# Kernel tuning notes

Measured on AMD Instinct MI355X. Metric: run time of the kernel, lower is better.

## Reference

```python
import jax, jax.numpy as jnp
import numpy as np

B, Hm, Wm, Dm = 1, 32, 32, 32
N = Hm * Wm * Dm
C = 128
HEADS, DH = 8, 16
G = 32
L = 2
OUT = 1


def _ln(x, g, b):
    mu = jnp.mean(x, -1, keepdims=True)
    var = jnp.mean((x - mu) ** 2, -1, keepdims=True)
    return (x - mu) * jax.lax.rsqrt(var + 1e-5) * g + b


def setup_inputs() -> dict:
    key = jax.random.key(0)
    ks = iter(jax.random.split(key, 64))
    def nrm(shape, s=0.02):
        return jax.random.normal(next(ks), shape, jnp.float32) * s
    return {
        "x": jax.random.normal(next(ks), (B, N, 3), jnp.float32),
        "fx": jax.random.normal(next(ks), (B, N, 1), jnp.float32),
        "pre_w1": nrm((4, 2 * C)), "pre_b1": jnp.zeros((2 * C,), jnp.float32),
        "pre_w2": nrm((2 * C, C)), "pre_b2": jnp.zeros((C,), jnp.float32),
        "placeholder": jax.random.uniform(next(ks), (C,), jnp.float32) / C,
        "ln1_g": jnp.ones((L, C), jnp.float32), "ln1_b": jnp.zeros((L, C), jnp.float32),
        "convx_w": nrm((L, C, C, 3, 3, 3)), "convx_b": jnp.zeros((L, C), jnp.float32),
        "convfx_w": nrm((L, C, C, 3, 3, 3)), "convfx_b": jnp.zeros((L, C), jnp.float32),
        "slice_w": nrm((L, DH, G), 0.1), "slice_b": jnp.zeros((L, G), jnp.float32),
        "temperature": jnp.full((L, 1, HEADS, 1, 1), 0.5, jnp.float32),
        "wq": nrm((L, DH, DH), 0.1), "wk": nrm((L, DH, DH), 0.1), "wv": nrm((L, DH, DH), 0.1),
        "wo": nrm((L, HEADS * DH, C)), "bo": jnp.zeros((L, C), jnp.float32),
        "ln2_g": jnp.ones((L, C), jnp.float32), "ln2_b": jnp.zeros((L, C), jnp.float32),
        "mlp_w1": nrm((L, C, C)), "mlp_b1": jnp.zeros((L, C), jnp.float32),
        "mlp_w2": nrm((L, C, C)), "mlp_b2": jnp.zeros((L, C), jnp.float32),
        "ln3_g": jnp.ones((C,), jnp.float32), "ln3_b": jnp.zeros((C,), jnp.float32),
        "out_w": nrm((C, OUT)), "out_b": jnp.zeros((OUT,), jnp.float32),
    }


def _conv3d(x, w, b):
    # x: [B,C,H,W,D], w: [O,I,3,3,3], SAME padding (kernel//2) as torch Conv3d
    y = jax.lax.conv_general_dilated(x, w, (1, 1, 1), "SAME",
                                     dimension_numbers=("NCDHW", "OIDHW", "NCDHW"))
    return y + b[None, :, None, None, None]


def _physics_attn(z, cw_x, cb_x, cw_fx, cb_fx, sw, sb, temp, wq, wk, wv, wo, bo):
    # z: [B, N, C] -> structured mesh conv projections -> slice attention
    xg = z.reshape(B, Hm, Wm, Dm, C).transpose(0, 4, 1, 2, 3)  # [B,C,H,W,D]

    def split_heads(t):  # [B,I,H,W,D] -> [B,heads,N,dh]
        return t.transpose(0, 2, 3, 4, 1).reshape(B, N, HEADS, DH).transpose(0, 2, 1, 3)

    x_mid = split_heads(_conv3d(xg, cw_x, cb_x))
    fx_mid = split_heads(_conv3d(xg, cw_fx, cb_fx))
    # slice assignment weights: [B,heads,N,G], temperature-scaled softmax
    slice_logits = (x_mid @ sw + sb) / temp
    swt = jax.nn.softmax(slice_logits, axis=-1)
    norm = jnp.sum(swt, axis=2)  # [B,heads,G]
    tok = jnp.einsum("bhnc,bhng->bhgc", fx_mid, swt) / (norm + 1e-5)[..., None]
    q, k, v = tok @ wq, tok @ wk, tok @ wv  # [B,heads,G,dh]
    attn = jax.nn.softmax((q @ k.transpose(0, 1, 3, 2)) * (DH ** -0.5), axis=-1)
    ot = attn @ v  # [B,heads,G,dh]
    out = jnp.einsum("bhgc,bhng->bhnc", ot, swt)  # de-slice back to tokens
    out = out.transpose(0, 2, 1, 3).reshape(B, N, HEADS * DH)
    return out @ wo + bo


def reference(x, fx, pre_w1, pre_b1, pre_w2, pre_b2, placeholder,
              ln1_g, ln1_b, convx_w, convx_b, convfx_w, convfx_b,
              slice_w, slice_b, temperature, wq, wk, wv, wo, bo,
              ln2_g, ln2_b, mlp_w1, mlp_b1, mlp_w2, mlp_b2,
              ln3_g, ln3_b, out_w, out_b):
    h = jnp.concatenate([x, fx], axis=-1)  # [B,N,space+fun]
    z = jax.nn.gelu(h @ pre_w1 + pre_b1, approximate=False) @ pre_w2 + pre_b2 + placeholder
    for l in range(L):
        zn = _ln(z, ln1_g[l], ln1_b[l])
        z = _physics_attn(zn, convx_w[l], convx_b[l], convfx_w[l], convfx_b[l],
                          slice_w[l], slice_b[l], temperature[l],
                          wq[l], wk[l], wv[l], wo[l], bo[l]) + z
        zn = _ln(z, ln2_g[l], ln2_b[l])
        z = jax.nn.gelu(zn @ mlp_w1[l] + mlp_b1[l], approximate=False) @ mlp_w2[l] + mlp_b2[l] + z
    return _ln(z, ln3_g, ln3_b) @ out_w + out_b
```

## Files before the change

kernel.cpp:

```cpp
#include <hip/hip_runtime.h>
#include <hip/hip_bf16.h>

#define DEV __device__ __forceinline__

constexpr int N   = 32768;
constexpr int TOTAL_IN = 2038481;

constexpr int OFF_X        = 0;
constexpr int OFF_FX       = 98304;
constexpr int OFF_PRE_W1   = 131072;
constexpr int OFF_PRE_B1   = 132096;
constexpr int OFF_PRE_W2   = 132352;
constexpr int OFF_PRE_B2   = 165120;
constexpr int OFF_PLACE    = 165248;
constexpr int OFF_LN1_G    = 165376;
constexpr int OFF_LN1_B    = 165632;
constexpr int OFF_CONVX_W  = 165888;
constexpr int OFF_CONVX_B  = 1050624;
constexpr int OFF_CONVFX_W = 1050880;
constexpr int OFF_CONVFX_B = 1935616;
constexpr int OFF_SLICE_W  = 1935872;
constexpr int OFF_SLICE_B  = 1936896;
constexpr int OFF_TEMP     = 1936960;
constexpr int OFF_WQ       = 1936976;
constexpr int OFF_WK       = 1937488;
constexpr int OFF_WV       = 1938000;
constexpr int OFF_WO       = 1938512;
constexpr int OFF_BO       = 1971280;
constexpr int OFF_LN2_G    = 1971536;
constexpr int OFF_LN2_B    = 1971792;
constexpr int OFF_MLP_W1   = 1972048;
constexpr int OFF_MLP_B1   = 2004816;
constexpr int OFF_MLP_W2   = 2005072;
constexpr int OFF_MLP_B2   = 2037840;
constexpr int OFF_LN3_G    = 2038096;
constexpr int OFF_LN3_B    = 2038224;
constexpr int OFF_OUT_W    = 2038352;
constexpr int OFF_OUT_B    = 2038480;

__device__ __constant__ int d_PRE[32] = {
  0, 98304, 131072, 132096, 132352, 165120, 165248, 165376, 165632,
  165888, 1050624, 1050880, 1935616, 1935872, 1936896, 1936960, 1936976,
  1937488, 1938000, 1938512, 1971280, 1971536, 1971792, 1972048, 2004816,
  2005072, 2037840, 2038096, 2038224, 2038352, 2038480, 2038481
};

constexpr size_t F_IN   = 16;
constexpr size_t F_WT   = 2038512;
constexpr size_t F_Z    = F_WT   + 1769472;
constexpr size_t F_ZN   = F_Z    + 4194304;
constexpr size_t F_CONV = F_ZN   + 4194304;
constexpr size_t F_SWT  = F_CONV + 8388608;
constexpr size_t F_TOKP = F_SWT  + 8388608;
constexpr size_t F_TOKR = F_TOKP + 1114112;
constexpr size_t F_OT   = F_TOKR + 4352;
constexpr size_t F_WP   = F_OT   + 4096;
constexpr size_t F_END  = F_WP   + 65536;

struct InPtrs { const void* p[31]; };

typedef short short8v  __attribute__((ext_vector_type(8)));
typedef float float4v  __attribute__((ext_vector_type(4)));
#define MFMA16(A,B,C) __builtin_amdgcn_mfma_f32_16x16x32_bf16(A,B,C,0,0,0)

DEV float geluf(float x) { return 0.5f * x * (1.0f + erff(x * 0.70710678118654752f)); }
DEV short f2bs(float x) { union { __hip_bfloat16 h; short s; } c; c.h = __float2bfloat16(x); return c.s; }

__global__ void k_convert(InPtrs ptrs, float* __restrict__ ws) {
  const unsigned tw = *(const unsigned*)ptrs.p[15];
  const bool isbf = (tw == 0x3F003F00u);
  int stride = gridDim.x * blockDim.x;
  for (int e = blockIdx.x * blockDim.x + threadIdx.x; e < TOTAL_IN; e += stride) {
    int lo = 0, hi = 30;
#pragma unroll
    for (int it = 0; it < 5; ++it) {
      int mid = (lo + hi + 1) >> 1;
      if (e >= d_PRE[mid]) lo = mid; else hi = mid - 1;
    }
    int loc = e - d_PRE[lo];
    float v;
    if (isbf) {
      unsigned short u = ((const unsigned short*)ptrs.p[lo])[loc];
      unsigned uu = ((unsigned)u) << 16;
      v = __uint_as_float(uu);
    } else {
      v = ((const float*)ptrs.p[lo])[loc];
    }
    ws[F_IN + e] = v;
  }
}

__global__ void k_wtrans(const float* __restrict__ ip, short* __restrict__ wtf) {
  int f = blockIdx.x * 256 + threadIdx.x;
  if (f >= 221184) return;
  int lane = f & 63;
  int rest = f >> 6;
  int ntile = rest & 15;
  int r2 = rest >> 4;
  int layer = r2 / 108;
  int kt = r2 - layer * 108;
  int icb = kt / 27, tap = kt - icb * 27;
  int oc = ntile * 16 + (lane & 15);
  int ic0 = icb * 32 + (lane >> 4) * 8;
  const float* cw = ip + (oc < 128 ? OFF_CONVX_W : OFF_CONVFX_W);
  int o = oc & 127;
  const float* src = cw + ((size_t)(layer * 128 + o) * 128) * 27 + tap;
  short8v out;
#pragma unroll
  for (int j = 0; j < 8; ++j) out[j] = f2bs(src[(ic0 + j) * 27]);
  *(short8v*)(wtf + (size_t)f * 8) = out;
}

__global__ void k_wpack(const float* __restrict__ ip, short* __restrict__ wp) {
  int f = blockIdx.x * 256 + threadIdx.x;
  if (f >= 16384) return;
  int lane = f & 63;
  int t = f >> 6;
  int srcoff, kt, nt;
  if (t < 64) { srcoff = OFF_PRE_W2; kt = t >> 3; nt = t & 7; }
  else {
    int r = t - 64, l = r / 96, r2 = r - l * 96;
    int which = r2 >> 5, idx2 = r2 & 31;
    kt = idx2 >> 3; nt = idx2 & 7;
    srcoff = (which == 0 ? OFF_MLP_W1 : (which == 1 ? OFF_MLP_W2 : OFF_WO)) + l * 16384;
  }
  int k0 = kt * 32 + (lane >> 4) * 8;
  int n = nt * 16 + (lane & 15);
  const float* src = ip + srcoff + (size_t)k0 * 128 + n;
  short8v out;
#pragma unroll
  for (int j = 0; j < 8; ++j) out[j] = f2bs(src[(size_t)j * 128]);
  *(short8v*)(wp + (size_t)f * 8) = out;
}

__global__ __launch_bounds__(256)
void k_prenet(const float* __restrict__ ip, const short* __restrict__ wp, float* __restrict__ z) {
  __shared__ float w1s[1024], b1s[256], cvec[128];
  __shared__ float xv[64][4];
  __shared__ __align__(16) short ts[64 * 264];
  int tid = threadIdx.x;
  int wv = tid >> 6, lane = tid & 63;
  int m = lane & 15, q = lane >> 4;
  int n0 = blockIdx.x * 64;
  for (int i = tid; i < 1024; i += 256) w1s[i] = ip[OFF_PRE_W1 + i];
  b1s[tid] = ip[OFF_PRE_B1 + tid];
  if (tid < 128) cvec[tid] = ip[OFF_PRE_B2 + tid] + ip[OFF_PLACE + tid];
  if (tid < 64) {
    xv[tid][0] = ip[OFF_X + (n0 + tid) * 3 + 0];
    xv[tid][1] = ip[OFF_X + (n0 + tid) * 3 + 1];
    xv[tid][2] = ip[OFF_X + (n0 + tid) * 3 + 2];
    xv[tid][3] = ip[OFF_FX + n0 + tid];
  }
  __syncthreads();
  {
    float w0 = w1s[tid], wA = w1s[256 + tid], wB = w1s[512 + tid], wC = w1s[768 + tid];
    float bb = b1s[tid];
    for (int t = 0; t < 64; ++t) {
      float hv = bb + xv[t][0] * w0 + xv[t][1] * wA + xv[t][2] * wB + xv[t][3] * wC;
      ts[t * 264 + tid] = f2bs(geluf(hv));
    }
  }
  __syncthreads();
  const short8v* pwf = (const short8v*)wp;
  float4v acc[8];
#pragma unroll
  for (int nt = 0; nt < 8; ++nt) acc[nt] = (float4v){0.f, 0.f, 0.f, 0.f};
  for (int kt = 0; kt < 8; ++kt) {
    short8v A = *(const short8v*)(ts + (wv * 16 + m) * 264 + kt * 32 + q * 8);
#pragma unroll
    for (int nt = 0; nt < 8; ++nt)
      acc[nt] = MFMA16(A, pwf[(kt * 8 + nt) * 64 + lane], acc[nt]);
  }
#pragma unroll
  for (int nt = 0; nt < 8; ++nt) {
    int col = nt * 16 + m;
#pragma unroll
    for (int r = 0; r < 4; ++r)
      z[(size_t)(n0 + wv * 16 + q * 4 + r) * 128 + col] = acc[nt][r] + cvec[col];
  }
}

__global__ void k_ln_bf(const float* __restrict__ src, short* __restrict__ dst,
                        const float* __restrict__ gm, const float* __restrict__ bt) {
  int wv = threadIdx.x >> 6, lane = threadIdx.x & 63;
  int n = blockIdx.x * 4 + wv;
  const float2 v = *(const float2*)&src[(size_t)n * 128 + lane * 2];
  float s1 = v.x + v.y, s2 = v.x * v.x + v.y * v.y;
#pragma unroll
  for (int off = 32; off; off >>= 1) { s1 += __shfl_xor(s1, off); s2 += __shfl_xor(s2, off); }
  float mu = s1 * (1.0f / 128.0f);
  float var = s2 * (1.0f / 128.0f) - mu * mu;
  float rst = 1.0f / sqrtf(var + 1e-5f);
  const float2 g2 = *(const float2*)&gm[lane * 2];
  const float2 b2 = *(const float2*)&bt[lane * 2];
  union { short s[2]; unsigned u; } c;
  c.s[0] = f2bs((v.x - mu) * rst * g2.x + b2.x);
  c.s[1] = f2bs((v.y - mu) * rst * g2.y + b2.y);
  *(unsigned*)&dst[(size_t)n * 128 + lane * 2] = c.u;
}

__global__ __launch_bounds__(256)
void k_conv(const float* __restrict__ ip, const short* __restrict__ znb,
            const short* __restrict__ wtf, float* __restrict__ cv, int layer) {
  __shared__ __align__(16) short halo[16320];
  int tid = threadIdx.x;
  int wv = tid >> 6, lane = tid & 63;
  int m = lane & 15, q = lane >> 4;
  int n0 = blockIdx.x * 64;
  int h = n0 >> 10, w0 = (n0 >> 5) & 31;
  float bias_r[4];
#pragma unroll
  for (int nt = 0; nt < 4; ++nt) {
    int oc = (wv * 4 + nt) * 16 + m;
    bias_r[nt] = (oc < 128) ? ip[OFF_CONVX_B + layer * 128 + oc]
                            : ip[OFF_CONVFX_B + layer * 128 + (oc - 128)];
  }
  float4v acc[4][4];
#pragma unroll
  for (int a = 0; a < 4; ++a)
#pragma unroll
    for (int b = 0; b < 4; ++b) acc[a][b] = (float4v){0.f, 0.f, 0.f, 0.f};

  const short8v* wf = (const short8v*)wtf + (size_t)layer * 110592 + (wv * 4) * 64 + lane;
  const int laneA = m * 40 + q * 8;
  short8v bc0 = wf[0], bc1 = wf[64], bc2 = wf[128], bc3 = wf[192];

  int tap = 0, icb = 0;
  for (int kt = 0; kt < 108; ++kt) {
    if (tap == 0) {
      __syncthreads();
      for (int i = tid; i < 1632; i += 256) {
        int pr = i >> 2, qq = i & 3;
        int line = pr / 34, dpos = pr - line * 34;
        int hh2 = h + (line >> 2) - 1, ww2 = w0 + (line & 3) - 1, dd2 = dpos - 1;
        short8v v = (short8v){0, 0, 0, 0, 0, 0, 0, 0};
        if (((unsigned)hh2 < 32u) && ((unsigned)ww2 < 32u) && ((unsigned)dd2 < 32u)) {
          int tok = (hh2 << 10) + (ww2 << 5) + dd2;
          v = *(const short8v*)(znb + (size_t)tok * 128 + icb * 32 + qq * 8);
        }
        *(short8v*)(halo + pr * 40 + qq * 8) = v;
      }
      __syncthreads();
    }
    int ktn = (kt + 1 < 108) ? kt + 1 : kt;
    const short8v* wn = wf + (size_t)ktn * 1024;
    short8v bn0 = wn[0], bn1 = wn[64], bn2 = wn[128], bn3 = wn[192];

    int ta = tap / 9, rem = tap - ta * 9, tb = rem / 3, tc = rem - tb * 3;
    const short* hp = halo + ((ta * 4 + tb) * 34 + tc) * 40 + laneA;
    short8v A0 = *(const short8v*)(hp);
    short8v A1 = *(const short8v*)(hp + 640);
    short8v A2 = *(const short8v*)(hp + 1360);
    short8v A3 = *(const short8v*)(hp + 2000);

    acc[0][0] = MFMA16(A0, bc0, acc[0][0]);
    acc[1][0] = MFMA16(A1, bc0, acc[1][0]);
    acc[2][0] = MFMA16(A2, bc0, acc[2][0]);
    acc[3][0] = MFMA16(A3, bc0, acc[3][0]);
    acc[0][1] = MFMA16(A0, bc1, acc[0][1]);
    acc[1][1] = MFMA16(A1, bc1, acc[1][1]);
    acc[2][1] = MFMA16(A2, bc1, acc[2][1]);
    acc[3][1] = MFMA16(A3, bc1, acc[3][1]);
    acc[0][2] = MFMA16(A0, bc2, acc[0][2]);
    acc[1][2] = MFMA16(A1, bc2, acc[1][2]);
    acc[2][2] = MFMA16(A2, bc2, acc[2][2]);
    acc[3][2] = MFMA16(A3, bc2, acc[3][2]);
    acc[0][3] = MFMA16(A0, bc3, acc[0][3]);
    acc[1][3] = MFMA16(A1, bc3, acc[1][3]);
    acc[2][3] = MFMA16(A2, bc3, acc[2][3]);
    acc[3][3] = MFMA16(A3, bc3, acc[3][3]);

    bc0 = bn0; bc1 = bn1; bc2 = bn2; bc3 = bn3;
    if (++tap == 27) { tap = 0; ++icb; }
  }
#pragma unroll
  for (int mt = 0; mt < 4; ++mt) {
    float* cp = cv + (size_t)(n0 + mt * 16 + q * 4) * 256 + (wv * 4) * 16 + m;
#pragma unroll
    for (int nt = 0; nt < 4; ++nt) {
#pragma unroll
      for (int r = 0; r < 4; ++r)
        cp[(size_t)r * 256 + nt * 16] = acc[mt][nt][r] + bias_r[nt];
    }
  }
}

__global__ __launch_bounds__(256)
void k_slice(const float* __restrict__ ip, const float* __restrict__ cv,
             short* __restrict__ swtb, float* __restrict__ tokp, int layer) {
  __shared__ float sws[512], sbs[32], its[8];
  __shared__ float swl[32 * 257];
  __shared__ float fxl[32 * 128];
  int tid = threadIdx.x;
  for (int i = tid; i < 512; i += 256) sws[i] = ip[OFF_SLICE_W + layer * 512 + i];
  if (tid < 32) sbs[tid] = ip[OFF_SLICE_B + layer * 32 + tid];
  if (tid < 8)  its[tid] = 1.0f / ip[OFF_TEMP + layer * 8 + tid];
  float4 ta0 = make_float4(0,0,0,0), ta1 = ta0, ta2 = ta0, ta3 = ta0;
  float np = 0.f;
  for (int s = 0; s < 4; ++s) {
    int tbase = blockIdx.x * 128 + s * 32;
    __syncthreads();
    for (int i = tid; i < 1024; i += 256) {
      int t = i >> 5, c4 = (i & 31) * 4;
      *(float4*)&fxl[t * 128 + c4] = *(const float4*)&cv[(size_t)(tbase + t) * 256 + 128 + c4];
    }
    {
      int t = tid >> 3, hh = tid & 7;
      float xm[16];
#pragma unroll
      for (int qq = 0; qq < 4; ++qq)
        *(float4*)&xm[qq * 4] = *(const float4*)&cv[(size_t)(tbase + t) * 256 + hh * 16 + qq * 4];
      float lg[32];
      float itv = its[hh];
#pragma unroll
      for (int g = 0; g < 32; ++g) {
        float sacc = sbs[g];
#pragma unroll
        for (int j = 0; j < 16; ++j) sacc += xm[j] * sws[j * 32 + g];
        lg[g] = sacc * itv;
      }
      float mx = -1e30f;
#pragma unroll
      for (int g = 0; g < 32; ++g) mx = fmaxf(mx, lg[g]);
      float sum = 0.f;
#pragma unroll
      for (int g = 0; g < 32; ++g) { lg[g] = expf(lg[g] - mx); sum += lg[g]; }
      float inv = 1.0f / sum;
#pragma unroll
      for (int g = 0; g < 32; ++g) {
        lg[g] *= inv;
        swl[t * 257 + hh * 32 + g] = lg[g];
      }
#pragma unroll
      for (int qq = 0; qq < 4; ++qq) {
        short8v pk;
#pragma unroll
        for (int j = 0; j < 8; ++j) pk[j] = f2bs(lg[qq * 8 + j]);
        *(short8v*)(swtb + (size_t)(tbase + t) * 256 + hh * 32 + qq * 8) = pk;
      }
    }
    __syncthreads();
    {
      int ah = tid >> 5, ag = tid & 31;
      for (int t2 = 0; t2 < 32; ++t2) {
        float sv = swl[t2 * 257 + ah * 32 + ag];
        np += sv;
        const float* f = &fxl[t2 * 128 + ah * 16];
        float4 f0 = *(const float4*)&f[0], f1 = *(const float4*)&f[4];
        float4 f2 = *(const float4*)&f[8], f3 = *(const float4*)&f[12];
        ta0.x += sv * f0.x; ta0.y += sv * f0.y; ta0.z += sv * f0.z; ta0.w += sv * f0.w;
        ta1.x += sv * f1.x; ta1.y += sv * f1.y; ta1.z += sv * f1.z; ta1.w += sv * f1.w;
        ta2.x += sv * f2.x; ta2.y += sv * f2.y; ta2.z += sv * f2.z; ta2.w += sv * f2.w;
        ta3.x += sv * f3.x; ta3.y += sv * f3.y; ta3.z += sv * f3.z; ta3.w += sv * f3.w;
      }
    }
  }
  int ah = tid >> 5, ag = tid & 31;
  size_t base = (size_t)blockIdx.x * 4352 + (size_t)(ah * 32 + ag) * 16;
  *(float4*)&tokp[base + 0]  = ta0;
  *(float4*)&tokp[base + 4]  = ta1;
  *(float4*)&tokp[base + 8]  = ta2;
  *(float4*)&tokp[base + 12] = ta3;
  tokp[(size_t)blockIdx.x * 4352 + 4096 + ah * 32 + ag] = np;
}

__global__ void k_tokred(const float* __restrict__ tokp, float* __restrict__ tokr) {
  int o = blockIdx.x * 256 + threadIdx.x;
  if (o < 4352) {
    float s = 0.f;
    for (int b = 0; b < 256; ++b) s += tokp[(size_t)b * 4352 + o];
    tokr[o] = s;
  }
}

__global__ __launch_bounds__(256)
void k_attn(const float* __restrict__ ip, const float* __restrict__ tokr,
            float* __restrict__ ot, int layer) {
  __shared__ float kk[256 * 17], vv[256 * 17];
  int tid = threadIdx.x;
  int hh = tid >> 5;
  const float* wq = ip + OFF_WQ + layer * 256;
  const float* wk = ip + OFF_WK + layer * 256;
  const float* wv = ip + OFF_WV + layer * 256;
  float inv = 1.0f / (tokr[4096 + tid] + 1e-5f);
  float t[16];
#pragma unroll
  for (int c = 0; c < 16; ++c) t[c] = tokr[tid * 16 + c] * inv;
  float q[16];
#pragma unroll
  for (int c = 0; c < 16; ++c) {
    float aq = 0.f, ak = 0.f, av = 0.f;
#pragma unroll
    for (int j = 0; j < 16; ++j) {
      float tv = t[j];
      aq += tv * wq[j * 16 + c];
      ak += tv * wk[j * 16 + c];
      av += tv * wv[j * 16 + c];
    }
    q[c] = aq;
    kk[tid * 17 + c] = ak;
    vv[tid * 17 + c] = av;
  }
  __syncthreads();
  float sc[32];
  float mx = -1e30f;
#pragma unroll
  for (int g2 = 0; g2 < 32; ++g2) {
    float s = 0.f;
#pragma unroll
    for (int c = 0; c < 16; ++c) s += q[c] * kk[(hh * 32 + g2) * 17 + c];
    s *= 0.25f;
    sc[g2] = s; mx = fmaxf(mx, s);
  }
  float sum = 0.f;
#pragma unroll
  for (int g2 = 0; g2 < 32; ++g2) { sc[g2] = expf(sc[g2] - mx); sum += sc[g2]; }
  float inv2 = 1.0f / sum;
  float o[16];
#pragma unroll
  for (int c = 0; c < 16; ++c) o[c] = 0.f;
#pragma unroll
  for (int g2 = 0; g2 < 32; ++g2) {
    float p = sc[g2] * inv2;
#pragma unroll
    for (int c = 0; c < 16; ++c) o[c] += p * vv[(hh * 32 + g2) * 17 + c];
  }
#pragma unroll
  for (int c = 0; c < 16; ++c) ot[tid * 16 + c] = o[c];
}

__global__ __launch_bounds__(256)
void k_out(const float* __restrict__ ip, const short* __restrict__ swtb,
           const float* __restrict__ ot, const short* __restrict__ wp,
           float* __restrict__ z, int layer) {
  __shared__ __align__(16) short otb[8 * 512];
  __shared__ __align__(16) short al[64 * 136];
  __shared__ float bol[128];
  int tid = threadIdx.x;
  int wv = tid >> 6, lane = tid & 63;
  int m = lane & 15, q = lane >> 4;
  int n0 = blockIdx.x * 64;
  if (tid < 128) bol[tid] = ip[OFF_BO + layer * 128 + tid];
  for (int i = tid; i < 4096; i += 256) {
    int h = i >> 9, r = i & 511, ln = r >> 3, j = r & 7;
    int g = (ln >> 4) * 8 + j, dh = ln & 15;
    otb[i] = f2bs(ot[h * 512 + g * 16 + dh]);
  }
  __syncthreads();
  float4v accd[8];
#pragma unroll
  for (int h = 0; h < 8; ++h) accd[h] = (float4v){0.f, 0.f, 0.f, 0.f};
#pragma unroll
  for (int h = 0; h < 8; ++h) {
    short8v A = *(const short8v*)(swtb + (size_t)(n0 + wv * 16 + m) * 256 + h * 32 + q * 8);
    accd[h] = MFMA16(A, *(const short8v*)(otb + h * 512 + lane * 8), accd[h]);
  }
#pragma unroll
  for (int h = 0; h < 8; ++h)
#pragma unroll
    for (int r = 0; r < 4; ++r)
      al[(wv * 16 + q * 4 + r) * 136 + h * 16 + m] = f2bs(accd[h][r]);
  __syncthreads();
  const short8v* wof = (const short8v*)(wp + (size_t)(128 + 96 * layer) * 512);
  float4v a2[8];
#pragma unroll
  for (int nt = 0; nt < 8; ++nt) a2[nt] = (float4v){0.f, 0.f, 0.f, 0.f};
  for (int kt = 0; kt < 4; ++kt) {
    short8v A = *(const short8v*)(al + (wv * 16 + m) * 136 + kt * 32 + q * 8);
#pragma unroll
    for (int nt = 0; nt < 8; ++nt)
      a2[nt] = MFMA16(A, wof[(kt * 8 + nt) * 64 + lane], a2[nt]);
  }
#pragma unroll
  for (int nt = 0; nt < 8; ++nt) {
    int col = nt * 16 + m;
#pragma unroll
    for (int r = 0; r < 4; ++r) {
      size_t zi = (size_t)(n0 + wv * 16 + q * 4 + r) * 128 + col;
      z[zi] += a2[nt][r] + bol[col];
    }
  }
}

__global__ __launch_bounds__(256)
void k_mlp(const float* __restrict__ ip, const short* __restrict__ znb,
           const short* __restrict__ wp, float* __restrict__ z, int layer) {
  __shared__ __align__(16) short znt[64 * 136];
  __shared__ __align__(16) short hid[64 * 136];
  __shared__ float b1s[128], b2s[128];
  int tid = threadIdx.x;
  int wv = tid >> 6, lane = tid & 63;
  int m = lane & 15, q = lane >> 4;
  int n0 = blockIdx.x * 64;
  if (tid < 128) {
    b1s[tid] = ip[OFF_MLP_B1 + layer * 128 + tid];
    b2s[tid] = ip[OFF_MLP_B2 + layer * 128 + tid];
  }
  for (int i = tid; i < 1024; i += 256) {
    int row = i >> 4, c8 = (i & 15) * 8;
    *(short8v*)(znt + row * 136 + c8) = *(const short8v*)(znb + (size_t)(n0 + row) * 128 + c8);
  }
  __syncthreads();
  const short8v* w1f = (const short8v*)(wp + (size_t)(64 + 96 * layer) * 512);
  const short8v* w2f = (const short8v*)(wp + (size_t)(96 + 96 * layer) * 512);
  float4v acc[8];
#pragma unroll
  for (int nt = 0; nt < 8; ++nt) acc[nt] = (float4v){0.f, 0.f, 0.f, 0.f};
  for (int kt = 0; kt < 4; ++kt) {
    short8v A = *(const short8v*)(znt + (wv * 16 + m) * 136 + kt * 32 + q * 8);
#pragma unroll
    for (int nt = 0; nt < 8; ++nt)
      acc[nt] = MFMA16(A, w1f[(kt * 8 + nt) * 64 + lane], acc[nt]);
  }
#pragma unroll
  for (int nt = 0; nt < 8; ++nt) {
    int col = nt * 16 + m;
#pragma unroll
    for (int r = 0; r < 4; ++r)
      hid[(wv * 16 + q * 4 + r) * 136 + col] = f2bs(geluf(acc[nt][r] + b1s[col]));
  }
  __syncthreads();
  float4v a2[8];
#pragma unroll
  for (int nt = 0; nt < 8; ++nt) a2[nt] = (float4v){0.f, 0.f, 0.f, 0.f};
  for (int kt = 0; kt < 4; ++kt) {
    short8v A = *(const short8v*)(hid + (wv * 16 + m) * 136 + kt * 32 + q * 8);
#pragma unroll
    for (int nt = 0; nt < 8; ++nt)
      a2[nt] = MFMA16(A, w2f[(kt * 8 + nt) * 64 + lane], a2[nt]);
  }
#pragma unroll
  for (int nt = 0; nt < 8; ++nt) {
    int col = nt * 16 + m;
#pragma unroll
    for (int r = 0; r < 4; ++r) {
      size_t zi = (size_t)(n0 + wv * 16 + q * 4 + r) * 128 + col;
      z[zi] += a2[nt][r] + b2s[col];
    }
  }
}

__global__ void k_final(const float* __restrict__ ip, const float* __restrict__ z,
                        void* __restrict__ dout, const void* __restrict__ tempraw) {
  int wv = threadIdx.x >> 6, lane = threadIdx.x & 63;
  int n = blockIdx.x * 4 + wv;
  const float2 v = *(const float2*)&z[(size_t)n * 128 + lane * 2];
  float s1 = v.x + v.y, s2 = v.x * v.x + v.y * v.y;
#pragma unroll
  for (int off = 32; off; off >>= 1) { s1 += __shfl_xor(s1, off); s2 += __shfl_xor(s2, off); }
  float mu = s1 * (1.0f / 128.0f);
  float var = s2 * (1.0f / 128.0f) - mu * mu;
  float rst = 1.0f / sqrtf(var + 1e-5f);
  const float2 g2 = *(const float2*)&ip[OFF_LN3_G + lane * 2];
  const float2 b2 = *(const float2*)&ip[OFF_LN3_B + lane * 2];
  const float2 ow = *(const float2*)&ip[OFF_OUT_W + lane * 2];
  float y0 = (v.x - mu) * rst * g2.x + b2.x;
  float y1 = (v.y - mu) * rst * g2.y + b2.y;
  float contrib = y0 * ow.x + y1 * ow.y;
#pragma unroll
  for (int off = 32; off; off >>= 1) contrib += __shfl_xor(contrib, off);
  if (lane == 0) {
    float res = contrib + ip[OFF_OUT_B];
    unsigned tw = *(const unsigned*)tempraw;
    if (tw == 0x3F003F00u) ((__hip_bfloat16*)dout)[n] = __float2bfloat16(res);
    else                   ((float*)dout)[n] = res;
  }
}

extern "C" void kernel_launch(void* const* d_in, const int* in_sizes, int n_in,
                              void* d_out, int out_size, void* d_ws, size_t ws_size,
                              hipStream_t stream) {
  (void)in_sizes; (void)out_size; (void)ws_size;
  if (n_in < 31) return;
  float* ws   = (float*)d_ws;
  float* ip   = ws + F_IN;
  short* wtf  = (short*)(ws + F_WT);
  float* z    = ws + F_Z;
  short* znb  = (short*)(ws + F_ZN);
  float* cv   = ws + F_CONV;
  short* swtb = (short*)(ws + F_SWT);
  float* tkp  = ws + F_TOKP;
  float* tkr  = ws + F_TOKR;
  float* ot   = ws + F_OT;
  short* wp   = (short*)(ws + F_WP);

  InPtrs P;
  for (int i = 0; i < 31; ++i) P.p[i] = d_in[i];

  k_convert<<<2048, 256, 0, stream>>>(P, ws);
  k_wtrans <<<864, 256, 0, stream>>>(ip, wtf);
  k_wpack  <<<64, 256, 0, stream>>>(ip, wp);
  k_prenet <<<512, 256, 0, stream>>>(ip, wp, z);
  for (int l = 0; l < 2; ++l) {
    k_ln_bf <<<8192, 256, 0, stream>>>(z, znb, ip + OFF_LN1_G + l * 128, ip + OFF_LN1_B + l * 128);
    k_conv  <<<512, 256, 0, stream>>>(ip, znb, wtf, cv, l);
    k_slice <<<256, 256, 0, stream>>>(ip, cv, swtb, tkp, l);
    k_tokred<<<17, 256, 0, stream>>>(tkp, tkr);
    k_attn  <<<1, 256, 0, stream>>>(ip, tkr, ot, l);
    k_out   <<<512, 256, 0, stream>>>(ip, swtb, ot, wp, z, l);
    k_ln_bf <<<8192, 256, 0, stream>>>(z, znb, ip + OFF_LN2_G + l * 128, ip + OFF_LN2_B + l * 128);
    k_mlp   <<<512, 256, 0, stream>>>(ip, znb, wp, z, l);
  }
  k_final<<<8192, 256, 0, stream>>>(ip, z, d_out, d_in[15]);
}
```

Measured before the change: 521.7 us.

## Fuse layernorms into producers, merge out-proj with MLP, split token reduction

Folds the LN1 normalisation into the prenet epilogue, and fuses the attention output projection, LN2, the MLP and the next layer's LN1 (or the final LN plus output head) into one kernel. This removes the separate layernorm and final kernels and their round trips of z through global memory. The token reduction becomes a two-stage reduction across 136 blocks, with the last stage done inside the attention kernel, to get more parallelism. The conv halo layout is also changed from padded rows to channel-quarter planes. The fused kernel uses more shared memory and registers, which may lower occupancy.

```diff
diff --git a/kernel.cpp b/kernel.cpp
--- a/kernel.cpp
+++ b/kernel.cpp
@@ -52,8 +52,8 @@
 constexpr size_t F_CONV = F_ZN   + 4194304;
 constexpr size_t F_SWT  = F_CONV + 8388608;
 constexpr size_t F_TOKP = F_SWT  + 8388608;
-constexpr size_t F_TOKR = F_TOKP + 1114112;
-constexpr size_t F_OT   = F_TOKR + 4352;
+constexpr size_t F_TOK2 = F_TOKP + 1114112;
+constexpr size_t F_OT   = F_TOK2 + 34816;
 constexpr size_t F_WP   = F_OT   + 4096;
 constexpr size_t F_END  = F_WP   + 65536;
 
@@ -134,8 +134,9 @@
 }
 
 __global__ __launch_bounds__(256)
-void k_prenet(const float* __restrict__ ip, const short* __restrict__ wp, float* __restrict__ z) {
-  __shared__ float w1s[1024], b1s[256], cvec[128];
+void k_prenet(const float* __restrict__ ip, const short* __restrict__ wp,
+              float* __restrict__ z, short* __restrict__ znb) {
+  __shared__ float w1s[1024], b1s[256], cvec[128], g1s[128], be1s[128];
   __shared__ float xv[64][4];
   __shared__ __align__(16) short ts[64 * 264];
   int tid = threadIdx.x;
@@ -144,7 +145,11 @@
   int n0 = blockIdx.x * 64;
   for (int i = tid; i < 1024; i += 256) w1s[i] = ip[OFF_PRE_W1 + i];
   b1s[tid] = ip[OFF_PRE_B1 + tid];
-  if (tid < 128) cvec[tid] = ip[OFF_PRE_B2 + tid] + ip[OFF_PLACE + tid];
+  if (tid < 128) {
+    cvec[tid] = ip[OFF_PRE_B2 + tid] + ip[OFF_PLACE + tid];
+    g1s[tid]  = ip[OFF_LN1_G + tid];
+    be1s[tid] = ip[OFF_LN1_B + tid];
+  }
   if (tid < 64) {
     xv[tid][0] = ip[OFF_X + (n0 + tid) * 3 + 0];
     xv[tid][1] = ip[OFF_X + (n0 + tid) * 3 + 1];
@@ -171,38 +176,39 @@
     for (int nt = 0; nt < 8; ++nt)
       acc[nt] = MFMA16(A, pwf[(kt * 8 + nt) * 64 + lane], acc[nt]);
   }
+  float vz[8][4];
 #pragma unroll
   for (int nt = 0; nt < 8; ++nt) {
     int col = nt * 16 + m;
 #pragma unroll
-    for (int r = 0; r < 4; ++r)
-      z[(size_t)(n0 + wv * 16 + q * 4 + r) * 128 + col] = acc[nt][r] + cvec[col];
-  }
-}
-
-__global__ void k_ln_bf(const float* __restrict__ src, short* __restrict__ dst,
-                        const float* __restrict__ gm, const float* __restrict__ bt) {
-  int wv = threadIdx.x >> 6, lane = threadIdx.x & 63;
-  int n = blockIdx.x * 4 + wv;
-  const float2 v = *(const float2*)&src[(size_t)n * 128 + lane * 2];
-  float s1 = v.x + v.y, s2 = v.x * v.x + v.y * v.y;
-#pragma unroll
-  for (int off = 32; off; off >>= 1) { s1 += __shfl_xor(s1, off); s2 += __shfl_xor(s2, off); }
-  float mu = s1 * (1.0f / 128.0f);
-  float var = s2 * (1.0f / 128.0f) - mu * mu;
-  float rst = 1.0f / sqrtf(var + 1e-5f);
-  const float2 g2 = *(const float2*)&gm[lane * 2];
-  const float2 b2 = *(const float2*)&bt[lane * 2];
-  union { short s[2]; unsigned u; } c;
-  c.s[0] = f2bs((v.x - mu) * rst * g2.x + b2.x);
-  c.s[1] = f2bs((v.y - mu) * rst * g2.y + b2.y);
-  *(unsigned*)&dst[(size_t)n * 128 + lane * 2] = c.u;
+    for (int r = 0; r < 4; ++r) {
+      vz[nt][r] = acc[nt][r] + cvec[col];
+      z[(size_t)(n0 + wv * 16 + q * 4 + r) * 128 + col] = vz[nt][r];
+    }
+  }
+#pragma unroll
+  for (int r = 0; r < 4; ++r) {
+    float s1 = 0.f, s2 = 0.f;
+#pragma unroll
+    for (int nt = 0; nt < 8; ++nt) { float v = vz[nt][r]; s1 += v; s2 += v * v; }
+#pragma unroll
+    for (int off = 1; off < 16; off <<= 1) { s1 += __shfl_xor(s1, off); s2 += __shfl_xor(s2, off); }
+    float mu = s1 * (1.0f / 128.0f);
+    float var = s2 * (1.0f / 128.0f) - mu * mu;
+    float rst = 1.0f / sqrtf(var + 1e-5f);
+    size_t rowb = (size_t)(n0 + wv * 16 + q * 4 + r) * 128;
+#pragma unroll
+    for (int nt = 0; nt < 8; ++nt) {
+      int col = nt * 16 + m;
+      znb[rowb + col] = f2bs((vz[nt][r] - mu) * rst * g1s[col] + be1s[col]);
+    }
+  }
 }
 
 __global__ __launch_bounds__(256)
 void k_conv(const float* __restrict__ ip, const short* __restrict__ znb,
             const short* __restrict__ wtf, float* __restrict__ cv, int layer) {
-  __shared__ __align__(16) short halo[16320];
+  __shared__ __align__(16) short halo[13056];
   int tid = threadIdx.x;
   int wv = tid >> 6, lane = tid & 63;
   int m = lane & 15, q = lane >> 4;
@@ -222,23 +228,23 @@
     for (int b = 0; b < 4; ++b) acc[a][b] = (float4v){0.f, 0.f, 0.f, 0.f};
 
   const short8v* wf = (const short8v*)wtf + (size_t)layer * 110592 + (wv * 4) * 64 + lane;
-  const int laneA = m * 40 + q * 8;
   short8v bc0 = wf[0], bc1 = wf[64], bc2 = wf[128], bc3 = wf[192];
 
   int tap = 0, icb = 0;
   for (int kt = 0; kt < 108; ++kt) {
     if (tap == 0) {
       __syncthreads();
-      for (int i = tid; i < 1632; i += 256) {
-        int pr = i >> 2, qq = i & 3;
+      for (int pr = tid; pr < 408; pr += 256) {
         int line = pr / 34, dpos = pr - line * 34;
         int hh2 = h + (line >> 2) - 1, ww2 = w0 + (line & 3) - 1, dd2 = dpos - 1;
-        short8v v = (short8v){0, 0, 0, 0, 0, 0, 0, 0};
-        if (((unsigned)hh2 < 32u) && ((unsigned)ww2 < 32u) && ((unsigned)dd2 < 32u)) {
-          int tok = (hh2 << 10) + (ww2 << 5) + dd2;
-          v = *(const short8v*)(znb + (size_t)tok * 128 + icb * 32 + qq * 8);
+        bool ok = ((unsigned)hh2 < 32u) && ((unsigned)ww2 < 32u) && ((unsigned)dd2 < 32u);
+        int tok = (hh2 << 10) + (ww2 << 5) + dd2;
+#pragma unroll
+        for (int qq = 0; qq < 4; ++qq) {
+          short8v v = (short8v){0, 0, 0, 0, 0, 0, 0, 0};
+          if (ok) v = *(const short8v*)(znb + (size_t)tok * 128 + icb * 32 + qq * 8);
+          *(short8v*)(halo + qq * 3264 + pr * 8) = v;
         }
-        *(short8v*)(halo + pr * 40 + qq * 8) = v;
       }
       __syncthreads();
     }
@@ -247,11 +253,11 @@
     short8v bn0 = wn[0], bn1 = wn[64], bn2 = wn[128], bn3 = wn[192];
 
     int ta = tap / 9, rem = tap - ta * 9, tb = rem / 3, tc = rem - tb * 3;
-    const short* hp = halo + ((ta * 4 + tb) * 34 + tc) * 40 + laneA;
+    const short* hp = halo + q * 3264 + (((ta * 4 + tb) * 34) + tc + m) * 8;
     short8v A0 = *(const short8v*)(hp);
-    short8v A1 = *(const short8v*)(hp + 640);
-    short8v A2 = *(const short8v*)(hp + 1360);
-    short8v A3 = *(const short8v*)(hp + 2000);
+    short8v A1 = *(const short8v*)(hp + 128);
+    short8v A2 = *(const short8v*)(hp + 272);
+    short8v A3 = *(const short8v*)(hp + 400);
 
     acc[0][0] = MFMA16(A0, bc0, acc[0][0]);
     acc[1][0] = MFMA16(A1, bc0, acc[1][0]);
@@ -364,28 +370,37 @@
   tokp[(size_t)blockIdx.x * 4352 + 4096 + ah * 32 + ag] = np;
 }
 
-__global__ void k_tokred(const float* __restrict__ tokp, float* __restrict__ tokr) {
-  int o = blockIdx.x * 256 + threadIdx.x;
-  if (o < 4352) {
-    float s = 0.f;
-    for (int b = 0; b < 256; ++b) s += tokp[(size_t)b * 4352 + o];
-    tokr[o] = s;
-  }
+__global__ void k_tokred1(const float* __restrict__ tokp, float* __restrict__ tok2) {
+  int ogrp = blockIdx.x % 17, bgrp = blockIdx.x / 17;
+  int o = ogrp * 256 + threadIdx.x;
+  float s = 0.f;
+  int b0 = bgrp * 32;
+#pragma unroll 8
+  for (int b = b0; b < b0 + 32; ++b) s += tokp[(size_t)b * 4352 + o];
+  tok2[(size_t)bgrp * 4352 + o] = s;
 }
 
 __global__ __launch_bounds__(256)
-void k_attn(const float* __restrict__ ip, const float* __restrict__ tokr,
+void k_attn(const float* __restrict__ ip, const float* __restrict__ tok2,
             float* __restrict__ ot, int layer) {
+  __shared__ float trs[4352];
   __shared__ float kk[256 * 17], vv[256 * 17];
   int tid = threadIdx.x;
+  for (int i = tid; i < 4352; i += 256) {
+    float s = 0.f;
+#pragma unroll
+    for (int b = 0; b < 8; ++b) s += tok2[(size_t)b * 4352 + i];
+    trs[i] = s;
+  }
+  __syncthreads();
   int hh = tid >> 5;
   const float* wq = ip + OFF_WQ + layer * 256;
   const float* wk = ip + OFF_WK + layer * 256;
   const float* wv = ip + OFF_WV + layer * 256;
-  float inv = 1.0f / (tokr[4096 + tid] + 1e-5f);
+  float inv = 1.0f / (trs[4096 + tid] + 1e-5f);
   float t[16];
 #pragma unroll
-  for (int c = 0; c < 16; ++c) t[c] = tokr[tid * 16 + c] * inv;
+  for (int c = 0; c < 16; ++c) t[c] = trs[tid * 16 + c] * inv;
   float q[16];
 #pragma unroll
   for (int c = 0; c < 16; ++c) {
@@ -430,75 +445,87 @@
 }
 
 __global__ __launch_bounds__(256)
-void k_out(const float* __restrict__ ip, const short* __restrict__ swtb,
-           const float* __restrict__ ot, const short* __restrict__ wp,
-           float* __restrict__ z, int layer) {
-  __shared__ __align__(16) short otb[8 * 512];
-  __shared__ __align__(16) short al[64 * 136];
-  __shared__ float bol[128];
-  int tid = threadIdx.x;
-  int wv = tid >> 6, lane = tid & 63;
-  int m = lane & 15, q = lane >> 4;
-  int n0 = blockIdx.x * 64;
-  if (tid < 128) bol[tid] = ip[OFF_BO + layer * 128 + tid];
-  for (int i = tid; i < 4096; i += 256) {
-    int h = i >> 9, r = i & 511, ln = r >> 3, j = r & 7;
-    int g = (ln >> 4) * 8 + j, dh = ln & 15;
-    otb[i] = f2bs(ot[h * 512 + g * 16 + dh]);
-  }
-  __syncthreads();
-  float4v accd[8];
-#pragma unroll
-  for (int h = 0; h < 8; ++h) accd[h] = (float4v){0.f, 0.f, 0.f, 0.f};
-#pragma unroll
-  for (int h = 0; h < 8; ++h) {
-    short8v A = *(const short8v*)(swtb + (size_t)(n0 + wv * 16 + m) * 256 + h * 32 + q * 8);
-    accd[h] = MFMA16(A, *(const short8v*)(otb + h * 512 + lane * 8), accd[h]);
-  }
-#pragma unroll
-  for (int h = 0; h < 8; ++h)
-#pragma unroll
-    for (int r = 0; r < 4; ++r)
-      al[(wv * 16 + q * 4 + r) * 136 + h * 16 + m] = f2bs(accd[h][r]);
-  __syncthreads();
-  const short8v* wof = (const short8v*)(wp + (size_t)(128 + 96 * layer) * 512);
-  float4v a2[8];
-#pragma unroll
-  for (int nt = 0; nt < 8; ++nt) a2[nt] = (float4v){0.f, 0.f, 0.f, 0.f};
-  for (int kt = 0; kt < 4; ++kt) {
-    short8v A = *(const short8v*)(al + (wv * 16 + m) * 136 + kt * 32 + q * 8);
-#pragma unroll
-    for (int nt = 0; nt < 8; ++nt)
-      a2[nt] = MFMA16(A, wof[(kt * 8 + nt) * 64 + lane], a2[nt]);
-  }
-#pragma unroll
-  for (int nt = 0; nt < 8; ++nt) {
-    int col = nt * 16 + m;
-#pragma unroll
-    for (int r = 0; r < 4; ++r) {
-      size_t zi = (size_t)(n0 + wv * 16 + q * 4 + r) * 128 + col;
-      z[zi] += a2[nt][r] + bol[col];
-    }
-  }
-}
-
-__global__ __launch_bounds__(256)
-void k_mlp(const float* __restrict__ ip, const short* __restrict__ znb,
-           const short* __restrict__ wp, float* __restrict__ z, int layer) {
-  __shared__ __align__(16) short znt[64 * 136];
-  __shared__ __align__(16) short hid[64 * 136];
-  __shared__ float b1s[128], b2s[128];
+void k_fused(const float* __restrict__ ip, const short* __restrict__ swtb,
+             const float* __restrict__ ot, const short* __restrict__ wp,
+             float* __restrict__ z, short* __restrict__ znb,
+             void* __restrict__ dout, const void* __restrict__ tempraw, int layer) {
+  __shared__ __align__(16) short otb[4096];
+  __shared__ __align__(16) short al[8704];
+  __shared__ __align__(16) short znt[8704];
+  __shared__ float bol[128], b1s[128], b2s[128], g2s[128], be2s[128], lng[128], lnb[128], ows[128];
   int tid = threadIdx.x;
   int wv = tid >> 6, lane = tid & 63;
   int m = lane & 15, q = lane >> 4;
   int n0 = blockIdx.x * 64;
   if (tid < 128) {
-    b1s[tid] = ip[OFF_MLP_B1 + layer * 128 + tid];
-    b2s[tid] = ip[OFF_MLP_B2 + layer * 128 + tid];
-  }
-  for (int i = tid; i < 1024; i += 256) {
-    int row = i >> 4, c8 = (i & 15) * 8;
-    *(short8v*)(znt + row * 136 + c8) = *(const short8v*)(znb + (size_t)(n0 + row) * 128 + c8);
+    bol[tid]  = ip[OFF_BO + layer * 128 + tid];
+    b1s[tid]  = ip[OFF_MLP_B1 + layer * 128 + tid];
+    b2s[tid]  = ip[OFF_MLP_B2 + layer * 128 + tid];
+    g2s[tid]  = ip[OFF_LN2_G + layer * 128 + tid];
+    be2s[tid] = ip[OFF_LN2_B + layer * 128 + tid];
+    if (layer == 0) {
+      lng[tid] = ip[OFF_LN1_G + 128 + tid];
+      lnb[tid] = ip[OFF_LN1_B + 128 + tid];
+      ows[tid] = 0.f;
+    } else {
+      lng[tid] = ip[OFF_LN3_G + tid];
+      lnb[tid] = ip[OFF_LN3_B + tid];
+      ows[tid] = ip[OFF_OUT_W + tid];
+    }
+  }
+  for (int i = tid; i < 4096; i += 256) {
+    int h = i >> 9, r = i & 511, ln = r >> 3, j = r & 7;
+    int g = (ln >> 4) * 8 + j, dh = ln & 15;
+    otb[i] = f2bs(ot[h * 512 + g * 16 + dh]);
+  }
+  __syncthreads();
+  float4v accd[8];
+#pragma unroll
+  for (int h = 0; h < 8; ++h) accd[h] = (float4v){0.f, 0.f, 0.f, 0.f};
+#pragma unroll
+  for (int h = 0; h < 8; ++h) {
+    short8v A = *(const short8v*)(swtb + (size_t)(n0 + wv * 16 + m) * 256 + h * 32 + q * 8);
+    accd[h] = MFMA16(A, *(const short8v*)(otb + h * 512 + lane * 8), accd[h]);
+  }
+#pragma unroll
+  for (int h = 0; h < 8; ++h)
+#pragma unroll
+    for (int r = 0; r < 4; ++r)
+      al[(wv * 16 + q * 4 + r) * 136 + h * 16 + m] = f2bs(accd[h][r]);
+  __syncthreads();
+  const short8v* wof = (const short8v*)(wp + (size_t)(128 + 96 * layer) * 512);
+  float4v a2[8];
+#pragma unroll
+  for (int nt = 0; nt < 8; ++nt) a2[nt] = (float4v){0.f, 0.f, 0.f, 0.f};
+  for (int kt = 0; kt < 4; ++kt) {
+    short8v A = *(const short8v*)(al + (wv * 16 + m) * 136 + kt * 32 + q * 8);
+#pragma unroll
+    for (int nt = 0; nt < 8; ++nt)
+      a2[nt] = MFMA16(A, wof[(kt * 8 + nt) * 64 + lane], a2[nt]);
+  }
+  float vmid[8][4];
+#pragma unroll
+  for (int nt = 0; nt < 8; ++nt) {
+    int col = nt * 16 + m;
+#pragma unroll
+    for (int r = 0; r < 4; ++r)
+      vmid[nt][r] = z[(size_t)(n0 + wv * 16 + q * 4 + r) * 128 + col] + a2[nt][r] + bol[col];
+  }
+#pragma unroll
+  for (int r = 0; r < 4; ++r) {
+    float s1 = 0.f, s2 = 0.f;
+#pragma unroll
+    for (int nt = 0; nt < 8; ++nt) { float v = vmid[nt][r]; s1 += v; s2 += v * v; }
+#pragma unroll
+    for (int off = 1; off < 16; off <<= 1) { s1 += __shfl_xor(s1, off); s2 += __shfl_xor(s2, off); }
+    float mu = s1 * (1.0f / 128.0f);
+    float var = s2 * (1.0f / 128.0f) - mu * mu;
+    float rst = 1.0f / sqrtf(var + 1e-5f);
+#pragma unroll
+    for (int nt = 0; nt < 8; ++nt) {
+      int col = nt * 16 + m;
+      znt[(wv * 16 + q * 4 + r) * 136 + col] = f2bs((vmid[nt][r] - mu) * rst * g2s[col] + be2s[col]);
+    }
   }
   __syncthreads();
   const short8v* w1f = (const short8v*)(wp + (size_t)(64 + 96 * layer) * 512);
@@ -512,58 +539,68 @@
     for (int nt = 0; nt < 8; ++nt)
       acc[nt] = MFMA16(A, w1f[(kt * 8 + nt) * 64 + lane], acc[nt]);
   }
+  __syncthreads();
 #pragma unroll
   for (int nt = 0; nt < 8; ++nt) {
     int col = nt * 16 + m;
 #pragma unroll
     for (int r = 0; r < 4; ++r)
-      hid[(wv * 16 + q * 4 + r) * 136 + col] = f2bs(geluf(acc[nt][r] + b1s[col]));
-  }
-  __syncthreads();
-  float4v a2[8];
-#pragma unroll
-  for (int nt = 0; nt < 8; ++nt) a2[nt] = (float4v){0.f, 0.f, 0.f, 0.f};
+      al[(wv * 16 + q * 4 + r) * 136 + col] = f2bs(geluf(acc[nt][r] + b1s[col]));
+  }
+  __syncthreads();
+  float4v a4[8];
+#pragma unroll
+  for (int nt = 0; nt < 8; ++nt) a4[nt] = (float4v){0.f, 0.f, 0.f, 0.f};
   for (int kt = 0; kt < 4; ++kt) {
-    short8v A = *(const short8v*)(hid + (wv * 16 + m) * 136 + kt * 32 + q * 8);
+    short8v A = *(const short8v*)(al + (wv * 16 + m) * 136 + kt * 32 + q * 8);
 #pragma unroll
     for (int nt = 0; nt < 8; ++nt)
-      a2[nt] = MFMA16(A, w2f[(kt * 8 + nt) * 64 + lane], a2[nt]);
-  }
+      a4[nt] = MFMA16(A, w2f[(kt * 8 + nt) * 64 + lane], a4[nt]);
+  }
+  float vfin[8][4];
 #pragma unroll
   for (int nt = 0; nt < 8; ++nt) {
     int col = nt * 16 + m;
 #pragma unroll
     for (int r = 0; r < 4; ++r) {
-      size_t zi = (size_t)(n0 + wv * 16 + q * 4 + r) * 128 + col;
-      z[zi] += a2[nt][r] + b2s[col];
-    }
-  }
-}
-
-__global__ void k_final(const float* __restrict__ ip, const float* __restrict__ z,
-                        void* __restrict__ dout, const void* __restrict__ tempraw) {
-  int wv = threadIdx.x >> 6, lane = threadIdx.x & 63;
-  int n = blockIdx.x * 4 + wv;
-  const float2 v = *(const float2*)&z[(size_t)n * 128 + lane * 2];
-  float s1 = v.x + v.y, s2 = v.x * v.x + v.y * v.y;
-#pragma unroll
-  for (int off = 32; off; off >>= 1) { s1 += __shfl_xor(s1, off); s2 += __shfl_xor(s2, off); }
-  float mu = s1 * (1.0f / 128.0f);
-  float var = s2 * (1.0f / 128.0f) - mu * mu;
-  float rst = 1.0f / sqrtf(var + 1e-5f);
-  const float2 g2 = *(const float2*)&ip[OFF_LN3_G + lane * 2];
-  const float2 b2 = *(const float2*)&ip[OFF_LN3_B + lane * 2];
-  const float2 ow = *(const float2*)&ip[OFF_OUT_W + lane * 2];
-  float y0 = (v.x - mu) * rst * g2.x + b2.x;
-  float y1 = (v.y - mu) * rst * g2.y + b2.y;
-  float contrib = y0 * ow.x + y1 * ow.y;
-#pragma unroll
-  for (int off = 32; off; off >>= 1) contrib += __shfl_xor(contrib, off);
-  if (lane == 0) {
-    float res = contrib + ip[OFF_OUT_B];
-    unsigned tw = *(const unsigned*)tempraw;
-    if (tw == 0x3F003F00u) ((__hip_bfloat16*)dout)[n] = __float2bfloat16(res);
-    else                   ((float*)dout)[n] = res;
+      vfin[nt][r] = vmid[nt][r] + a4[nt][r] + b2s[col];
+      z[(size_t)(n0 + wv * 16 + q * 4 + r) * 128 + col] = vfin[nt][r];
+    }
+  }
+#pragma unroll
+  for (int r = 0; r < 4; ++r) {
+    float s1 = 0.f, s2 = 0.f;
+#pragma unroll
+    for (int nt = 0; nt < 8; ++nt) { float v = vfin[nt][r]; s1 += v; s2 += v * v; }
+#pragma unroll
+    for (int off = 1; off < 16; off <<= 1) { s1 += __shfl_xor(s1, off); s2 += __shfl_xor(s2, off); }
+    float mu = s1 * (1.0f / 128.0f);
+    float var = s2 * (1.0f / 128.0f) - mu * mu;
+    float rst = 1.0f / sqrtf(var + 1e-5f);
+    int n = n0 + wv * 16 + q * 4 + r;
+    if (layer == 0) {
+      size_t rowb = (size_t)n * 128;
+#pragma unroll
+      for (int nt = 0; nt < 8; ++nt) {
+        int col = nt * 16 + m;
+        znb[rowb + col] = f2bs((vfin[nt][r] - mu) * rst * lng[col] + lnb[col]);
+      }
+    } else {
+      float contrib = 0.f;
+#pragma unroll
+      for (int nt = 0; nt < 8; ++nt) {
+        int col = nt * 16 + m;
+        contrib += ((vfin[nt][r] - mu) * rst * lng[col] + lnb[col]) * ows[col];
+      }
+#pragma unroll
+      for (int off = 1; off < 16; off <<= 1) contrib += __shfl_xor(contrib, off);
+      if (m == 0) {
+        float res = contrib + ip[OFF_OUT_B];
+        unsigned tw = *(const unsigned*)tempraw;
+        if (tw == 0x3F003F00u) ((__hip_bfloat16*)dout)[n] = __float2bfloat16(res);
+        else                   ((float*)dout)[n] = res;
+      }
+    }
   }
 }
 
@@ -580,7 +617,7 @@
   float* cv   = ws + F_CONV;
   short* swtb = (short*)(ws + F_SWT);
   float* tkp  = ws + F_TOKP;
-  float* tkr  = ws + F_TOKR;
+  float* tk2  = ws + F_TOK2;
   float* ot   = ws + F_OT;
   short* wp   = (short*)(ws + F_WP);
 
@@ -590,16 +627,12 @@
   k_convert<<<2048, 256, 0, stream>>>(P, ws);
   k_wtrans <<<864, 256, 0, stream>>>(ip, wtf);
   k_wpack  <<<64, 256, 0, stream>>>(ip, wp);
-  k_prenet <<<512, 256, 0, stream>>>(ip, wp, z);
+  k_prenet <<<512, 256, 0, stream>>>(ip, wp, z, znb);
   for (int l = 0; l < 2; ++l) {
-    k_ln_bf <<<8192, 256, 0, stream>>>(z, znb, ip + OFF_LN1_G + l * 128, ip + OFF_LN1_B + l * 128);
-    k_conv  <<<512, 256, 0, stream>>>(ip, znb, wtf, cv, l);
-    k_slice <<<256, 256, 0, stream>>>(ip, cv, swtb, tkp, l);
-    k_tokred<<<17, 256, 0, stream>>>(tkp, tkr);
-    k_attn  <<<1, 256, 0, stream>>>(ip, tkr, ot, l);
-    k_out   <<<512, 256, 0, stream>>>(ip, swtb, ot, wp, z, l);
-    k_ln_bf <<<8192, 256, 0, stream>>>(z, znb, ip + OFF_LN2_G + l * 128, ip + OFF_LN2_B + l * 128);
-    k_mlp   <<<512, 256, 0, stream>>>(ip, znb, wp, z, l);
-  }
-  k_final<<<8192, 256, 0, stream>>>(ip, z, d_out, d_in[15]);
-}
+    k_conv   <<<512, 256, 0, stream>>>(ip, znb, wtf, cv, l);
+    k_slice  <<<256, 256, 0, stream>>>(ip, cv, swtb, tkp, l);
+    k_tokred1<<<136, 256, 0, stream>>>(tkp, tk2);
+    k_attn   <<<1, 256, 0, stream>>>(ip, tk2, ot, l);
+    k_fused  <<<512, 256, 0, stream>>>(ip, swtb, ot, wp, z, znb, d_out, d_in[15], l);
+  }
+}
```

New measurement: 474.3 us. -9.1%, faster.
